# Optimization experiments

Measured on AMD Instinct MI355X. Metric: run time of the kernel, lower is better.

Reference implementation:

```python
import jax, jax.numpy as jnp
import numpy as np

WS = 7   # window size
SS = 3   # shift size


def _ln(x, g, b):
    m = x.mean(-1, keepdims=True)
    v = ((x - m) ** 2).mean(-1, keepdims=True)
    return (x - m) / jnp.sqrt(v + 1e-5) * g + b


def setup_inputs() -> dict:
    key = jax.random.key(0)
    ks = jax.random.split(key, 8)
    B, H, W, C, nh = 64, 56, 56, 96, 3
    N = WS * WS
    x = jax.random.normal(ks[0], (B, H * W, C), jnp.float32)

    # Swin SW-MSA attention mask: [nW, N, N], 0 where attention is allowed, -100 otherwise
    img = np.zeros((H, W), np.int32)
    cnt = 0
    for hs in (slice(0, H - WS), slice(H - WS, H - SS), slice(H - SS, None)):
        for wsl in (slice(0, W - WS), slice(W - WS, W - SS), slice(W - SS, None)):
            img[hs, wsl] = cnt
            cnt += 1
    win = img.reshape(H // WS, WS, W // WS, WS).transpose(0, 2, 1, 3).reshape(-1, N)
    am = np.where(win[:, None, :] != win[:, :, None], -100.0, 0.0).astype(np.float32)

    # relative position index: [N, N] in [0, (2*WS-1)^2)
    coords = np.stack(np.meshgrid(np.arange(WS), np.arange(WS), indexing='ij')).reshape(2, -1)
    rel = (coords[:, :, None] - coords[:, None, :]).transpose(1, 2, 0)
    rel[..., 0] += WS - 1
    rel[..., 1] += WS - 1
    rel[..., 0] *= 2 * WS - 1
    rel_index = jnp.asarray(rel.sum(-1), jnp.int32)

    p = lambda k, sh: jax.random.normal(k, sh, jnp.float32) * 0.02
    return dict(
        x=x,
        attn_mask=jnp.asarray(am),
        rel_index=rel_index,
        norm1_g=jnp.ones((C,), jnp.float32), norm1_b=jnp.zeros((C,), jnp.float32),
        qkv_w=p(ks[1], (3 * C, C)), qkv_b=jnp.zeros((3 * C,), jnp.float32),
        rel_bias_table=p(ks[2], ((2 * WS - 1) ** 2, nh)),
        proj_w=p(ks[3], (C, C)), proj_b=jnp.zeros((C,), jnp.float32),
        norm2_g=jnp.ones((C,), jnp.float32), norm2_b=jnp.zeros((C,), jnp.float32),
        fc1_w=p(ks[4], (4 * C, C)), fc1_b=jnp.zeros((4 * C,), jnp.float32),
        fc2_w=p(ks[5], (C, 4 * C)), fc2_b=jnp.zeros((C,), jnp.float32),
        H=56, W=56,
    )


def reference(x, attn_mask, rel_index, norm1_g, norm1_b, qkv_w, qkv_b,
              rel_bias_table, proj_w, proj_b, norm2_g, norm2_b,
              fc1_w, fc1_b, fc2_w, fc2_b, H, W):
    B, L, C = x.shape
    nh = rel_bias_table.shape[1]
    d = C // nh
    N = WS * WS
    shortcut = x

    xn = _ln(x, norm1_g, norm1_b).reshape(B, H, W, C)
    # cyclic shift (H%WS==0, W%WS==0 so no padding needed)
    xs = jnp.roll(xn, (-SS, -SS), axis=(1, 2))
    # window partition -> [B*nW, N, C]
    xw = xs.reshape(B, H // WS, WS, W // WS, WS, C).transpose(0, 1, 3, 2, 4, 5).reshape(-1, N, C)
    B_ = xw.shape[0]
    nW = attn_mask.shape[0]

    qkv = (xw @ qkv_w.T + qkv_b).reshape(B_, N, 3, nh, d).transpose(2, 0, 3, 1, 4)
    q, k, v = qkv[0] * (d ** -0.5), qkv[1], qkv[2]  # [B_, nh, N, d]
    attn = jnp.einsum('bhnd,bhmd->bhnm', q, k)
    bias = rel_bias_table[rel_index.reshape(-1)].reshape(N, N, nh).transpose(2, 0, 1)
    attn = attn + bias[None]
    attn = attn.reshape(B_ // nW, nW, nh, N, N) + attn_mask[None, :, None]
    attn = jax.nn.softmax(attn.reshape(B_, nh, N, N), axis=-1)
    out = jnp.einsum('bhnm,bhmd->bhnd', attn, v).transpose(0, 2, 1, 3).reshape(B_, N, C)
    out = out @ proj_w.T + proj_b

    # window reverse + reverse cyclic shift
    xr = out.reshape(B, H // WS, W // WS, WS, WS, C).transpose(0, 1, 3, 2, 4, 5).reshape(B, H, W, C)
    xr = jnp.roll(xr, (SS, SS), axis=(1, 2)).reshape(B, L, C)

    x = shortcut + xr
    h = _ln(x, norm2_g, norm2_b)
    h = jax.nn.gelu(h @ fc1_w.T + fc1_b, approximate=False) @ fc2_w.T + fc2_b
    return x + h
```

## Files before the change

### kernel.cpp

```cpp
#include <hip/hip_runtime.h>
#include <hip/hip_bf16.h>

typedef __attribute__((ext_vector_type(8))) short short8;
typedef __attribute__((ext_vector_type(4))) float f32x4;

constexpr int HW = 56;

constexpr int SR    = 104;
constexpr int SVT   = 200;
constexpr int OFF_X = 0;
constexpr int OFF_Q = 64 * SR;
constexpr int OFF_K = 2 * 64 * SR;
constexpr int OFF_V = 3 * 64 * SR;
constexpr int POOLN = OFF_V + 32 * SVT;

constexpr int WQKV  = 0;
constexpr int WPROJ = 27648;
constexpr int WFC1  = 36864;
constexpr int WFC2  = 73728;
constexpr int WTOT  = 110592;
constexpr int BIASN = 64 * 3 * 49 * 64;
constexpr size_t WS_M1 = (size_t)WTOT * 2;
constexpr size_t WS_M2 = WS_M1 + (size_t)BIASN * 4;

__device__ __forceinline__ ushort bfc(float f) {
  union { __hip_bfloat16 h; ushort u; } v;
  v.h = __float2bfloat16(f);
  return v.u;
}
__device__ __forceinline__ uint pk2(float a, float b) {
  union { __hip_bfloat162 h2; uint u; } v;
  v.h2 = __float22bfloat162_rn(make_float2(a, b));
  return v.u;
}
__device__ __forceinline__ void st4(short* p, float a, float b, float c, float d) {
  uint2 u; u.x = pk2(a, b); u.y = pk2(c, d);
  *(uint2*)p = u;
}
__device__ __forceinline__ short8 ldw8(const float* p) {
  float4 a = *(const float4*)p;
  float4 b = *(const float4*)(p + 4);
  short8 r;
  r[0] = (short)bfc(a.x); r[1] = (short)bfc(a.y); r[2] = (short)bfc(a.z); r[3] = (short)bfc(a.w);
  r[4] = (short)bfc(b.x); r[5] = (short)bfc(b.y); r[6] = (short)bfc(b.z); r[7] = (short)bfc(b.w);
  return r;
}
template<bool PRE>
__device__ __forceinline__ short8 wfrag(const short* wsb, int ts, int lane, const float* fsrc) {
  if constexpr (PRE) return *(const short8*)&wsb[(ts << 9) + lane * 8];
  else               return ldw8(fsrc);
}
__device__ __forceinline__ float gelu(float v) {
  return v * __builtin_amdgcn_rcpf(1.0f + __expf(-1.702f * v));
}
__device__ __forceinline__ void stage9(const short* g0, short* l0, int wv, int lane) {
  #pragma unroll
  for (int s4 = 0; s4 < 3; ++s4) {
    int s = wv + 4 * s4;
    if (s < 9)
      __builtin_amdgcn_global_load_lds((const unsigned int*)(g0 + (s << 9) + lane * 8),
                                       (unsigned int*)(l0 + (s << 9)), 16, 0, 0);
  }
}

__global__ __launch_bounds__(256) void cvt_weights(
    const float* __restrict__ qkv_w, const float* __restrict__ proj_w,
    const float* __restrict__ fc1_w, const float* __restrict__ fc2_w,
    short* __restrict__ ws)
{
  int idx = blockIdx.x * 256 + threadIdx.x;
  if (idx >= WTOT) return;
  int j = idx & 7, lane = (idx >> 3) & 63;
  int cl = lane & 15;
  int g  = 8 * (lane >> 4) + j;
  float v;
  if (idx < WPROJ) {
    int ts = idx >> 9; int tile = ts / 3, s = ts - 3 * tile;
    v = qkv_w[(size_t)(16 * tile + cl) * 96 + 32 * s + g];
    if (tile < 6) v *= 0.17677669529663687f;
  } else if (idx < WFC1) {
    int ts = (idx - WPROJ) >> 9; int tile = ts / 3, s = ts - 3 * tile;
    v = proj_w[(size_t)(16 * tile + cl) * 96 + 32 * s + g];
  } else if (idx < WFC2) {
    int ts = (idx - WFC1) >> 9; int T = ts / 3, s = ts - 3 * T;
    int cn = T / 6, nt = T - 6 * cn;
    v = fc1_w[(size_t)(96 * cn + 16 * nt + cl) * 96 + 32 * s + g];
  } else {
    int ts = (idx - WFC2) >> 9; int T = ts / 3, s = ts - 3 * T;
    int cn = T / 6, nt = T - 6 * cn;
    v = fc2_w[(size_t)(16 * nt + cl) * 384 + 96 * cn + 32 * s + g];
  }
  ws[idx] = (short)bfc(v);
}

__global__ __launch_bounds__(256) void prep_bias(
    const float* __restrict__ attn_mask, const int* __restrict__ rel_index,
    const float* __restrict__ rel_tab, float* __restrict__ bias3)
{
  int idx = blockIdx.x * 256 + threadIdx.x;
  if (idx >= BIASN) return;
  int k = idx & 63;
  int t = idx >> 6;
  int q = t % 49;
  int wh = t / 49;
  int h = wh % 3, w = wh / 3;
  float v = -1e30f;
  if (k < 49) {
    int qk = q * 49 + k;
    v = rel_tab[rel_index[qk] * 3 + h] + attn_mask[(size_t)w * 2401 + qk];
  }
  bias3[idx] = v;
}

template<int MODE>
__global__ __launch_bounds__(256, 3) void swin_mfma_kernel(
    const float* __restrict__ x,
    const float* __restrict__ attn_mask,
    const int*   __restrict__ rel_index,
    const float* __restrict__ n1g, const float* __restrict__ n1b,
    const float* __restrict__ qkv_w, const float* __restrict__ qkv_b,
    const float* __restrict__ rel_tab,
    const float* __restrict__ proj_w, const float* __restrict__ proj_b,
    const float* __restrict__ n2g, const float* __restrict__ n2b,
    const float* __restrict__ fc1_w, const float* __restrict__ fc1_b,
    const float* __restrict__ fc2_w, const float* __restrict__ fc2_b,
    const short* __restrict__ wsw,
    const float* __restrict__ bias3,
    float* __restrict__ out)
{
  constexpr bool PRE = (MODE >= 1);
  __shared__ alignas(16) short pool[POOLN];
  short* bufA = (short*)&pool[OFF_K];
  short* bufB = (short*)&pool[OFF_K + 4608];

  const int tid  = threadIdx.x;
  const int wv   = tid >> 6;
  const int lane = tid & 63;
  const int ln   = lane & 15;
  const int gq   = lane >> 4;
  const int bw   = blockIdx.x;
  const int b    = bw >> 6, widx = bw & 63;
  const int wr   = widx >> 3, wc = widx & 7;

  const f32x4 zf = {0.f, 0.f, 0.f, 0.f};
  const int qq = 16 * wv + ln;

  auto gbase = [&](int n) -> size_t {
    int i = n / 7, j = n - 7 * i;
    int h = wr * 7 + i + 3; if (h >= HW) h -= HW;
    int w = wc * 7 + j + 3; if (w >= HW) w -= HW;
    return ((size_t)b * (HW * HW) + (size_t)h * HW + w) * 96;
  };
  const size_t obase = gbase(qq < 49 ? qq : 48);

  float xraw[6][4];
  {
    if (qq < 49) {
      const float* xr = x + obase;
      #pragma unroll
      for (int nt = 0; nt < 6; ++nt) {
        float4 v = *(const float4*)&xr[16 * nt + 4 * gq];
        xraw[nt][0] = v.x; xraw[nt][1] = v.y; xraw[nt][2] = v.z; xraw[nt][3] = v.w;
      }
    } else {
      #pragma unroll
      for (int nt = 0; nt < 6; ++nt)
        xraw[nt][0] = xraw[nt][1] = xraw[nt][2] = xraw[nt][3] = 0.f;
    }
    float s1 = 0.f, s2 = 0.f;
    #pragma unroll
    for (int nt = 0; nt < 6; ++nt)
      #pragma unroll
      for (int r = 0; r < 4; ++r) { s1 += xraw[nt][r]; s2 += xraw[nt][r] * xraw[nt][r]; }
    s1 += __shfl_xor(s1, 16, 64); s1 += __shfl_xor(s1, 32, 64);
    s2 += __shfl_xor(s2, 16, 64); s2 += __shfl_xor(s2, 32, 64);
    float mean = s1 * (1.f / 96.f);
    float inv  = rsqrtf(s2 * (1.f / 96.f) - mean * mean + 1e-5f);
    #pragma unroll
    for (int nt = 0; nt < 6; ++nt) {
      float4 g4 = *(const float4*)&n1g[16 * nt + 4 * gq];
      float4 b4 = *(const float4*)&n1b[16 * nt + 4 * gq];
      st4(&pool[OFF_X + qq * SR + 16 * nt + 4 * gq],
          (xraw[nt][0] - mean) * inv * g4.x + b4.x,
          (xraw[nt][1] - mean) * inv * g4.y + b4.y,
          (xraw[nt][2] - mean) * inv * g4.z + b4.z,
          (xraw[nt][3] - mean) * inv * g4.w + b4.w);
    }
  }
  __syncthreads();

  {
    short8 af[3][4];
    #pragma unroll
    for (int s = 0; s < 3; ++s)
      #pragma unroll
      for (int m = 0; m < 4; ++m)
        af[s][m] = *(const short8*)&pool[OFF_X + (16 * m + ln) * SR + 32 * s + 8 * gq];

    const float sc_ = 0.17677669529663687f;
    for (int t = wv; t < 18; t += 4) {
      short8 wf[3];
      #pragma unroll
      for (int s = 0; s < 3; ++s)
        wf[s] = wfrag<PRE>(wsw + WQKV, t * 3 + s, lane,
                           qkv_w + (size_t)(16 * t + ln) * 96 + 32 * s + 8 * gq);
      int which = t / 6;
      if (which == 2) {
        int d  = 16 * (t - 12) + ln;
        float bv = qkv_b[192 + d];
        int dd = d & 31, hh = d >> 5;
        __builtin_amdgcn_s_setprio(1);
        #pragma unroll
        for (int m = 0; m < 4; ++m) {
          f32x4 acc = zf;
          #pragma unroll
          for (int s = 0; s < 3; ++s)
            acc = __builtin_amdgcn_mfma_f32_16x16x32_bf16(af[s][m], wf[s], acc, 0, 0, 0);
          st4(&pool[OFF_V + dd * SVT + hh * 64 + 16 * m + 4 * gq],
              acc[0] + bv, acc[1] + bv, acc[2] + bv, acc[3] + bv);
        }
        __builtin_amdgcn_s_setprio(0);
      } else {
        float4 b4 = *(const float4*)&qkv_b[16 * t + 4 * gq];
        if (which == 0) {
          if constexpr (PRE) { b4.x *= sc_; b4.y *= sc_; b4.z *= sc_; b4.w *= sc_; }
        }
        __builtin_amdgcn_s_setprio(1);
        #pragma unroll
        for (int m = 0; m < 4; ++m) {
          f32x4 acc = zf;
          #pragma unroll
          for (int s = 0; s < 3; ++s)
            acc = __builtin_amdgcn_mfma_f32_16x16x32_bf16(wf[s], af[s][m], acc, 0, 0, 0);
          int tok = 16 * m + ln;
          float v0 = acc[0] + b4.x, v1 = acc[1] + b4.y, v2 = acc[2] + b4.z, v3 = acc[3] + b4.w;
          if (which == 0) {
            if constexpr (PRE)
              st4(&pool[OFF_Q + tok * SR + 16 * t + 4 * gq], v0, v1, v2, v3);
            else
              st4(&pool[OFF_Q + tok * SR + 16 * t + 4 * gq], v0 * sc_, v1 * sc_, v2 * sc_, v3 * sc_);
          } else {
            st4(&pool[OFF_K + tok * SR + 16 * (t - 6) + 4 * gq], v0, v1, v2, v3);
          }
        }
        __builtin_amdgcn_s_setprio(0);
      }
    }
  }
  __syncthreads();

  const int qc = qq < 49 ? qq : 48;
  int   relvv[4][4];
  float maskb[4][4];
  if constexpr (MODE < 2) {
    #pragma unroll
    for (int nt = 0; nt < 4; ++nt)
      #pragma unroll
      for (int r = 0; r < 4; ++r) {
        int key = 16 * nt + 4 * gq + r;
        if (key < 49) {
          int qk = qc * 49 + key;
          relvv[nt][r] = rel_index[qk];
          maskb[nt][r] = attn_mask[(size_t)widx * 2401 + qk];
        } else {
          relvv[nt][r] = 0;
          maskb[nt][r] = -1e30f;
        }
      }
  }
  const float* bph = nullptr;
  if constexpr (MODE == 2) bph = bias3 + ((size_t)widx * 3 * 49 + qc) * 64;

  for (int h = 0; h < 3; ++h) {
    short8 bq = *(const short8*)&pool[OFF_Q + qq * SR + h * 32 + 8 * gq];
    f32x4 sc[4];
    __builtin_amdgcn_s_setprio(1);
    #pragma unroll
    for (int nt = 0; nt < 4; ++nt) {
      f32x4 bia;
      if constexpr (MODE == 2) {
        bia = *(const f32x4*)&bph[h * 3136 + 16 * nt + 4 * gq];
      } else {
        #pragma unroll
        for (int r = 0; r < 4; ++r)
          bia[r] = rel_tab[relvv[nt][r] * 3 + h] + maskb[nt][r];
      }
      short8 ak = *(const short8*)&pool[OFF_K + (16 * nt + ln) * SR + h * 32 + 8 * gq];
      sc[nt] = __builtin_amdgcn_mfma_f32_16x16x32_bf16(ak, bq, bia, 0, 0, 0);
    }
    __builtin_amdgcn_s_setprio(0);
    float pv[4][4];
    float sum = 0.f;
    #pragma unroll
    for (int nt = 0; nt < 4; ++nt)
      #pragma unroll
      for (int r = 0; r < 4; ++r) { pv[nt][r] = __expf(sc[nt][r]); sum += pv[nt][r]; }
    sum += __shfl_xor(sum, 16, 64);
    sum += __shfl_xor(sum, 32, 64);
    float inv = __builtin_amdgcn_rcpf(sum);
    #pragma unroll
    for (int nt = 0; nt < 4; ++nt)
      st4(&pool[OFF_X + qq * SR + 16 * nt + 4 * gq],
          pv[nt][0] * inv, pv[nt][1] * inv, pv[nt][2] * inv, pv[nt][3] * inv);

    short8 bp0 = *(const short8*)&pool[OFF_X + qq * SR + 8 * gq];
    short8 bp1 = *(const short8*)&pool[OFF_X + qq * SR + 32 + 8 * gq];
    __builtin_amdgcn_s_setprio(1);
    #pragma unroll
    for (int dt = 0; dt < 2; ++dt) {
      short8 av0 = *(const short8*)&pool[OFF_V + (16 * dt + ln) * SVT + h * 64 + 8 * gq];
      short8 av1 = *(const short8*)&pool[OFF_V + (16 * dt + ln) * SVT + h * 64 + 32 + 8 * gq];
      f32x4 o = __builtin_amdgcn_mfma_f32_16x16x32_bf16(av0, bp0, zf, 0, 0, 0);
      o = __builtin_amdgcn_mfma_f32_16x16x32_bf16(av1, bp1, o, 0, 0, 0);
      st4(&pool[OFF_Q + qq * SR + h * 32 + 16 * dt + 4 * gq], o[0], o[1], o[2], o[3]);
    }
    __builtin_amdgcn_s_setprio(0);
  }

  short8 ao[3];
  #pragma unroll
  for (int s = 0; s < 3; ++s)
    ao[s] = *(const short8*)&pool[OFF_Q + qq * SR + 32 * s + 8 * gq];
  __syncthreads();

  if constexpr (PRE) stage9(wsw + WPROJ, bufA, wv, lane);
  __syncthreads();

  if constexpr (PRE) stage9(wsw + WPROJ + 9 * 512, bufB, wv, lane);
  float y[6][4];
  __builtin_amdgcn_s_setprio(1);
  #pragma unroll
  for (int nt = 0; nt < 3; ++nt) {
    f32x4 acc = zf;
    #pragma unroll
    for (int s = 0; s < 3; ++s) {
      short8 wfr = PRE ? *(const short8*)&bufA[(nt * 3 + s) * 512 + lane * 8]
                       : ldw8(proj_w + (size_t)(16 * nt + ln) * 96 + 32 * s + 8 * gq);
      acc = __builtin_amdgcn_mfma_f32_16x16x32_bf16(wfr, ao[s], acc, 0, 0, 0);
    }
    float4 pb = *(const float4*)&proj_b[16 * nt + 4 * gq];
    y[nt][0] = acc[0] + pb.x + xraw[nt][0];
    y[nt][1] = acc[1] + pb.y + xraw[nt][1];
    y[nt][2] = acc[2] + pb.z + xraw[nt][2];
    y[nt][3] = acc[3] + pb.w + xraw[nt][3];
  }
  __builtin_amdgcn_s_setprio(0);
  __syncthreads();

  if constexpr (PRE) stage9(wsw + WFC1, bufA, wv, lane);
  __builtin_amdgcn_s_setprio(1);
  #pragma unroll
  for (int nt = 3; nt < 6; ++nt) {
    f32x4 acc = zf;
    #pragma unroll
    for (int s = 0; s < 3; ++s) {
      short8 wfr = PRE ? *(const short8*)&bufB[((nt - 3) * 3 + s) * 512 + lane * 8]
                       : ldw8(proj_w + (size_t)(16 * nt + ln) * 96 + 32 * s + 8 * gq);
      acc = __builtin_amdgcn_mfma_f32_16x16x32_bf16(wfr, ao[s], acc, 0, 0, 0);
    }
    float4 pb = *(const float4*)&proj_b[16 * nt + 4 * gq];
    y[nt][0] = acc[0] + pb.x + xraw[nt][0];
    y[nt][1] = acc[1] + pb.y + xraw[nt][1];
    y[nt][2] = acc[2] + pb.z + xraw[nt][2];
    y[nt][3] = acc[3] + pb.w + xraw[nt][3];
  }
  __builtin_amdgcn_s_setprio(0);
  {
    float s1 = 0.f, s2 = 0.f;
    #pragma unroll
    for (int nt = 0; nt < 6; ++nt)
      #pragma unroll
      for (int r = 0; r < 4; ++r) { s1 += y[nt][r]; s2 += y[nt][r] * y[nt][r]; }
    s1 += __shfl_xor(s1, 16, 64); s1 += __shfl_xor(s1, 32, 64);
    s2 += __shfl_xor(s2, 16, 64); s2 += __shfl_xor(s2, 32, 64);
    float mean = s1 * (1.f / 96.f);
    float inv  = rsqrtf(s2 * (1.f / 96.f) - mean * mean + 1e-5f);
    #pragma unroll
    for (int nt = 0; nt < 6; ++nt) {
      float4 g4 = *(const float4*)&n2g[16 * nt + 4 * gq];
      float4 b4 = *(const float4*)&n2b[16 * nt + 4 * gq];
      st4(&pool[OFF_Q + qq * SR + 16 * nt + 4 * gq],
          (y[nt][0] - mean) * inv * g4.x + b4.x,
          (y[nt][1] - mean) * inv * g4.y + b4.y,
          (y[nt][2] - mean) * inv * g4.z + b4.z,
          (y[nt][3] - mean) * inv * g4.w + b4.w);
    }
  }
  short8 ay[3];
  #pragma unroll
  for (int s = 0; s < 3; ++s)
    ay[s] = *(const short8*)&pool[OFF_Q + qq * SR + 32 * s + 8 * gq];
  __syncthreads();

  f32x4 accO[6] = {zf, zf, zf, zf, zf, zf};
  for (int cn = 0; cn < 4; ++cn) {
    if constexpr (PRE) stage9(wsw + WFC1 + (cn * 18 + 9) * 512, bufB, wv, lane);
    __builtin_amdgcn_s_setprio(1);
    #pragma unroll
    for (int nt = 0; nt < 3; ++nt) {
      f32x4 acc = zf;
      #pragma unroll
      for (int s = 0; s < 3; ++s) {
        short8 wfr = PRE ? *(const short8*)&bufA[(nt * 3 + s) * 512 + lane * 8]
                         : ldw8(fc1_w + (size_t)(96 * cn + 16 * nt + ln) * 96 + 32 * s + 8 * gq);
        acc = __builtin_amdgcn_mfma_f32_16x16x32_bf16(wfr, ay[s], acc, 0, 0, 0);
      }
      float4 b1 = *(const float4*)&fc1_b[96 * cn + 16 * nt + 4 * gq];
      st4(&pool[OFF_X + qq * SR + 16 * nt + 4 * gq],
          gelu(acc[0] + b1.x), gelu(acc[1] + b1.y),
          gelu(acc[2] + b1.z), gelu(acc[3] + b1.w));
    }
    __builtin_amdgcn_s_setprio(0);
    __syncthreads();
    if constexpr (PRE) stage9(wsw + WFC2 + (cn * 18) * 512, bufA, wv, lane);
    __builtin_amdgcn_s_setprio(1);
    #pragma unroll
    for (int nt = 3; nt < 6; ++nt) {
      f32x4 acc = zf;
      #pragma unroll
      for (int s = 0; s < 3; ++s) {
        short8 wfr = PRE ? *(const short8*)&bufB[((nt - 3) * 3 + s) * 512 + lane * 8]
                         : ldw8(fc1_w + (size_t)(96 * cn + 16 * nt + ln) * 96 + 32 * s + 8 * gq);
        acc = __builtin_amdgcn_mfma_f32_16x16x32_bf16(wfr, ay[s], acc, 0, 0, 0);
      }
      float4 b1 = *(const float4*)&fc1_b[96 * cn + 16 * nt + 4 * gq];
      st4(&pool[OFF_X + qq * SR + 16 * nt + 4 * gq],
          gelu(acc[0] + b1.x), gelu(acc[1] + b1.y),
          gelu(acc[2] + b1.z), gelu(acc[3] + b1.w));
    }
    __builtin_amdgcn_s_setprio(0);
    short8 ah[3];
    #pragma unroll
    for (int s = 0; s < 3; ++s)
      ah[s] = *(const short8*)&pool[OFF_X + qq * SR + 32 * s + 8 * gq];
    __syncthreads();
    if constexpr (PRE) stage9(wsw + WFC2 + (cn * 18 + 9) * 512, bufB, wv, lane);
    __builtin_amdgcn_s_setprio(1);
    #pragma unroll
    for (int nt = 0; nt < 3; ++nt) {
      #pragma unroll
      for (int s = 0; s < 3; ++s) {
        short8 wfr = PRE ? *(const short8*)&bufA[(nt * 3 + s) * 512 + lane * 8]
                         : ldw8(fc2_w + (size_t)(16 * nt + ln) * 384 + 96 * cn + 32 * s + 8 * gq);
        accO[nt] = __builtin_amdgcn_mfma_f32_16x16x32_bf16(wfr, ah[s], accO[nt], 0, 0, 0);
      }
    }
    __builtin_amdgcn_s_setprio(0);
    __syncthreads();
    if constexpr (PRE) { if (cn < 3) stage9(wsw + WFC1 + ((cn + 1) * 18) * 512, bufA, wv, lane); }
    __builtin_amdgcn_s_setprio(1);
    #pragma unroll
    for (int nt = 3; nt < 6; ++nt) {
      #pragma unroll
      for (int s = 0; s < 3; ++s) {
        short8 wfr = PRE ? *(const short8*)&bufB[((nt - 3) * 3 + s) * 512 + lane * 8]
                         : ldw8(fc2_w + (size_t)(16 * nt + ln) * 384 + 96 * cn + 32 * s + 8 * gq);
        accO[nt] = __builtin_amdgcn_mfma_f32_16x16x32_bf16(wfr, ah[s], accO[nt], 0, 0, 0);
      }
    }
    __builtin_amdgcn_s_setprio(0);
    __syncthreads();
  }

  if (qq < 49) {
    float* dst = out + obase;
    #pragma unroll
    for (int nt = 0; nt < 6; ++nt) {
      float4 fb = *(const float4*)&fc2_b[16 * nt + 4 * gq];
      float4 v;
      v.x = y[nt][0] + accO[nt][0] + fb.x;
      v.y = y[nt][1] + accO[nt][1] + fb.y;
      v.z = y[nt][2] + accO[nt][2] + fb.z;
      v.w = y[nt][3] + accO[nt][3] + fb.w;
      *(float4*)&dst[16 * nt + 4 * gq] = v;
    }
  }
}

extern "C" void kernel_launch(void* const* d_in, const int* in_sizes, int n_in,
                              void* d_out, int out_size, void* d_ws, size_t ws_size,
                              hipStream_t stream) {
  const float* x         = (const float*)d_in[0];
  const float* attn_mask = (const float*)d_in[1];
  const int*   rel_index = (const int*)  d_in[2];
  const float* n1g       = (const float*)d_in[3];
  const float* n1b       = (const float*)d_in[4];
  const float* qkv_w     = (const float*)d_in[5];
  const float* qkv_b     = (const float*)d_in[6];
  const float* rel_tab   = (const float*)d_in[7];
  const float* proj_w    = (const float*)d_in[8];
  const float* proj_b    = (const float*)d_in[9];
  const float* n2g       = (const float*)d_in[10];
  const float* n2b       = (const float*)d_in[11];
  const float* fc1_w     = (const float*)d_in[12];
  const float* fc1_b     = (const float*)d_in[13];
  const float* fc2_w     = (const float*)d_in[14];
  const float* fc2_b     = (const float*)d_in[15];
  float* out = (float*)d_out;

  const int B = in_sizes[0] / (HW * HW * 96);
  const bool m1 = ws_size >= WS_M1;
  const bool m2 = ws_size >= WS_M2;
  short* ws    = (short*)d_ws;
  float* bias3 = (float*)((char*)d_ws + WS_M1);

  if (m1)
    cvt_weights<<<(WTOT + 255) / 256, 256, 0, stream>>>(qkv_w, proj_w, fc1_w, fc2_w, ws);
  if (m2)
    prep_bias<<<(BIASN + 255) / 256, 256, 0, stream>>>(attn_mask, rel_index, rel_tab, bias3);

  if (m2)
    swin_mfma_kernel<2><<<B * 64, 256, 0, stream>>>(
        x, attn_mask, rel_index, n1g, n1b, qkv_w, qkv_b, rel_tab, proj_w, proj_b,
        n2g, n2b, fc1_w, fc1_b, fc2_w, fc2_b, (const short*)ws, (const float*)bias3, out);
  else if (m1)
    swin_mfma_kernel<1><<<B * 64, 256, 0, stream>>>(
        x, attn_mask, rel_index, n1g, n1b, qkv_w, qkv_b, rel_tab, proj_w, proj_b,
        n2g, n2b, fc1_w, fc1_b, fc2_w, fc2_b, (const short*)ws, (const float*)nullptr, out);
  else
    swin_mfma_kernel<0><<<B * 64, 256, 0, stream>>>(
        x, attn_mask, rel_index, n1g, n1b, qkv_w, qkv_b, rel_tab, proj_w, proj_b,
        n2g, n2b, fc1_w, fc1_b, fc2_w, fc2_b, (const short*)nullptr, (const float*)nullptr, out);
}
```

Measured before the change: 155.9 us.

## Repack MFMA outputs via shuffles and double-buffer full 18-tile weight stages

Replaces the LDS round trip for the softmax probabilities and the GELU hidden activations with in-register cross-lane shuffles that rebuild the bf16 B-operand fragments directly. Weight staging moves from 9-tile half buffers to full 18-tile buffers placed at two LDS regions, with each stage prefetching the next layer's weights. Each MLP chunk now runs FC1 and FC2 as whole phases, roughly halving the __syncthreads count. This trades LDS traffic and barriers for extra shuffle instructions and higher register pressure from holding six accumulators and the repacked fragments.

```diff
diff --git a/kernel.cpp b/kernel.cpp
--- a/kernel.cpp
+++ b/kernel.cpp
@@ -13,6 +13,10 @@
 constexpr int OFF_K = 2 * 64 * SR;
 constexpr int OFF_V = 3 * 64 * SR;
 constexpr int POOLN = OFF_V + 32 * SVT;
+constexpr int BUF0  = 0;
+constexpr int BUF1  = 9216;
+constexpr int YN    = OFF_V;
+constexpr int YSTR  = 96;
 
 constexpr int WQKV  = 0;
 constexpr int WPROJ = 27648;
@@ -53,11 +57,26 @@
 __device__ __forceinline__ float gelu(float v) {
   return v * __builtin_amdgcn_rcpf(1.0f + __expf(-1.702f * v));
 }
-__device__ __forceinline__ void stage9(const short* g0, short* l0, int wv, int lane) {
+__device__ __forceinline__ short8 repack(f32x4 A, f32x4 B, int ln, int gq) {
+  uint a_lo = pk2(A[0], A[1]), a_hi = pk2(A[2], A[3]);
+  uint b_lo = pk2(B[0], B[1]), b_hi = pk2(B[2], B[3]);
+  int s0 = ln + (((2 * gq)     & 3) << 4);
+  int s1 = ln + (((2 * gq + 1) & 3) << 4);
+  uint A0 = __shfl(a_lo, s0, 64), B0 = __shfl(b_lo, s0, 64);
+  uint A1 = __shfl(a_hi, s0, 64), B1 = __shfl(b_hi, s0, 64);
+  uint A2 = __shfl(a_lo, s1, 64), B2 = __shfl(b_lo, s1, 64);
+  uint A3 = __shfl(a_hi, s1, 64), B3 = __shfl(b_hi, s1, 64);
+  bool uA = (gq < 2);
+  union { uint u[4]; short8 s8; } r;
+  r.u[0] = uA ? A0 : B0; r.u[1] = uA ? A1 : B1;
+  r.u[2] = uA ? A2 : B2; r.u[3] = uA ? A3 : B3;
+  return r.s8;
+}
+__device__ __forceinline__ void stage18(const short* g0, short* l0, int wv, int lane) {
   #pragma unroll
-  for (int s4 = 0; s4 < 3; ++s4) {
-    int s = wv + 4 * s4;
-    if (s < 9)
+  for (int i = 0; i < 5; ++i) {
+    int s = wv + 4 * i;
+    if (s < 18)
       __builtin_amdgcn_global_load_lds((const unsigned int*)(g0 + (s << 9) + lane * 8),
                                        (unsigned int*)(l0 + (s << 9)), 16, 0, 0);
   }
@@ -130,8 +149,8 @@
 {
   constexpr bool PRE = (MODE >= 1);
   __shared__ alignas(16) short pool[POOLN];
-  short* bufA = (short*)&pool[OFF_K];
-  short* bufB = (short*)&pool[OFF_K + 4608];
+  short* buf0 = pool + BUF0;
+  short* buf1 = pool + BUF1;
 
   const int tid  = threadIdx.x;
   const int wv   = tid >> 6;
@@ -289,7 +308,7 @@
       sc[nt] = __builtin_amdgcn_mfma_f32_16x16x32_bf16(ak, bq, bia, 0, 0, 0);
     }
     __builtin_amdgcn_s_setprio(0);
-    float pv[4][4];
+    f32x4 pv[4];
     float sum = 0.f;
     #pragma unroll
     for (int nt = 0; nt < 4; ++nt)
@@ -300,11 +319,10 @@
     float inv = __builtin_amdgcn_rcpf(sum);
     #pragma unroll
     for (int nt = 0; nt < 4; ++nt)
-      st4(&pool[OFF_X + qq * SR + 16 * nt + 4 * gq],
-          pv[nt][0] * inv, pv[nt][1] * inv, pv[nt][2] * inv, pv[nt][3] * inv);
-
-    short8 bp0 = *(const short8*)&pool[OFF_X + qq * SR + 8 * gq];
-    short8 bp1 = *(const short8*)&pool[OFF_X + qq * SR + 32 + 8 * gq];
+      #pragma unroll
+      for (int r = 0; r < 4; ++r) pv[nt][r] *= inv;
+    short8 bp0 = repack(pv[0], pv[1], ln, gq);
+    short8 bp1 = repack(pv[2], pv[3], ln, gq);
     __builtin_amdgcn_s_setprio(1);
     #pragma unroll
     for (int dt = 0; dt < 2; ++dt) {
@@ -323,18 +341,18 @@
     ao[s] = *(const short8*)&pool[OFF_Q + qq * SR + 32 * s + 8 * gq];
   __syncthreads();
 
-  if constexpr (PRE) stage9(wsw + WPROJ, bufA, wv, lane);
+  if constexpr (PRE) stage18(wsw + WPROJ, buf0, wv, lane);
   __syncthreads();
 
-  if constexpr (PRE) stage9(wsw + WPROJ + 9 * 512, bufB, wv, lane);
+  if constexpr (PRE) stage18(wsw + WFC1, buf1, wv, lane);
   float y[6][4];
   __builtin_amdgcn_s_setprio(1);
   #pragma unroll
-  for (int nt = 0; nt < 3; ++nt) {
+  for (int nt = 0; nt < 6; ++nt) {
     f32x4 acc = zf;
     #pragma unroll
     for (int s = 0; s < 3; ++s) {
-      short8 wfr = PRE ? *(const short8*)&bufA[(nt * 3 + s) * 512 + lane * 8]
+      short8 wfr = PRE ? *(const short8*)&buf0[((nt * 3 + s) << 9) + lane * 8]
                        : ldw8(proj_w + (size_t)(16 * nt + ln) * 96 + 32 * s + 8 * gq);
       acc = __builtin_amdgcn_mfma_f32_16x16x32_bf16(wfr, ao[s], acc, 0, 0, 0);
     }
@@ -345,26 +363,6 @@
     y[nt][3] = acc[3] + pb.w + xraw[nt][3];
   }
   __builtin_amdgcn_s_setprio(0);
-  __syncthreads();
-
-  if constexpr (PRE) stage9(wsw + WFC1, bufA, wv, lane);
-  __builtin_amdgcn_s_setprio(1);
-  #pragma unroll
-  for (int nt = 3; nt < 6; ++nt) {
-    f32x4 acc = zf;
-    #pragma unroll
-    for (int s = 0; s < 3; ++s) {
-      short8 wfr = PRE ? *(const short8*)&bufB[((nt - 3) * 3 + s) * 512 + lane * 8]
-                       : ldw8(proj_w + (size_t)(16 * nt + ln) * 96 + 32 * s + 8 * gq);
-      acc = __builtin_amdgcn_mfma_f32_16x16x32_bf16(wfr, ao[s], acc, 0, 0, 0);
-    }
-    float4 pb = *(const float4*)&proj_b[16 * nt + 4 * gq];
-    y[nt][0] = acc[0] + pb.x + xraw[nt][0];
-    y[nt][1] = acc[1] + pb.y + xraw[nt][1];
-    y[nt][2] = acc[2] + pb.z + xraw[nt][2];
-    y[nt][3] = acc[3] + pb.w + xraw[nt][3];
-  }
-  __builtin_amdgcn_s_setprio(0);
   {
     float s1 = 0.f, s2 = 0.f;
     #pragma unroll
@@ -379,7 +377,7 @@
     for (int nt = 0; nt < 6; ++nt) {
       float4 g4 = *(const float4*)&n2g[16 * nt + 4 * gq];
       float4 b4 = *(const float4*)&n2b[16 * nt + 4 * gq];
-      st4(&pool[OFF_Q + qq * SR + 16 * nt + 4 * gq],
+      st4(&pool[YN + qq * YSTR + 16 * nt + 4 * gq],
           (y[nt][0] - mean) * inv * g4.x + b4.x,
           (y[nt][1] - mean) * inv * g4.y + b4.y,
           (y[nt][2] - mean) * inv * g4.z + b4.z,
@@ -389,77 +387,49 @@
   short8 ay[3];
   #pragma unroll
   for (int s = 0; s < 3; ++s)
-    ay[s] = *(const short8*)&pool[OFF_Q + qq * SR + 32 * s + 8 * gq];
+    ay[s] = *(const short8*)&pool[YN + qq * YSTR + 32 * s + 8 * gq];
   __syncthreads();
 
   f32x4 accO[6] = {zf, zf, zf, zf, zf, zf};
+  short8 hq[3];
+  #pragma unroll
   for (int cn = 0; cn < 4; ++cn) {
-    if constexpr (PRE) stage9(wsw + WFC1 + (cn * 18 + 9) * 512, bufB, wv, lane);
+    if constexpr (PRE) stage18(wsw + WFC2 + (cn * 18) * 512, buf0, wv, lane);
+    f32x4 ha[6];
     __builtin_amdgcn_s_setprio(1);
     #pragma unroll
-    for (int nt = 0; nt < 3; ++nt) {
+    for (int nt = 0; nt < 6; ++nt) {
       f32x4 acc = zf;
       #pragma unroll
       for (int s = 0; s < 3; ++s) {
-        short8 wfr = PRE ? *(const short8*)&bufA[(nt * 3 + s) * 512 + lane * 8]
+        short8 wfr = PRE ? *(const short8*)&buf1[((nt * 3 + s) << 9) + lane * 8]
                          : ldw8(fc1_w + (size_t)(96 * cn + 16 * nt + ln) * 96 + 32 * s + 8 * gq);
         acc = __builtin_amdgcn_mfma_f32_16x16x32_bf16(wfr, ay[s], acc, 0, 0, 0);
       }
       float4 b1 = *(const float4*)&fc1_b[96 * cn + 16 * nt + 4 * gq];
-      st4(&pool[OFF_X + qq * SR + 16 * nt + 4 * gq],
-          gelu(acc[0] + b1.x), gelu(acc[1] + b1.y),
-          gelu(acc[2] + b1.z), gelu(acc[3] + b1.w));
+      ha[nt][0] = gelu(acc[0] + b1.x);
+      ha[nt][1] = gelu(acc[1] + b1.y);
+      ha[nt][2] = gelu(acc[2] + b1.z);
+      ha[nt][3] = gelu(acc[3] + b1.w);
     }
     __builtin_amdgcn_s_setprio(0);
+    #pragma unroll
+    for (int s = 0; s < 3; ++s) hq[s] = repack(ha[2 * s], ha[2 * s + 1], ln, gq);
     __syncthreads();
-    if constexpr (PRE) stage9(wsw + WFC2 + (cn * 18) * 512, bufA, wv, lane);
+
+    if constexpr (PRE) { if (cn < 3) stage18(wsw + WFC1 + ((cn + 1) * 18) * 512, buf1, wv, lane); }
     __builtin_amdgcn_s_setprio(1);
     #pragma unroll
-    for (int nt = 3; nt < 6; ++nt) {
-      f32x4 acc = zf;
+    for (int nt = 0; nt < 6; ++nt) {
       #pragma unroll
       for (int s = 0; s < 3; ++s) {
-        short8 wfr = PRE ? *(const short8*)&bufB[((nt - 3) * 3 + s) * 512 + lane * 8]
-                         : ldw8(fc1_w + (size_t)(96 * cn + 16 * nt + ln) * 96 + 32 * s + 8 * gq);
-        acc = __builtin_amdgcn_mfma_f32_16x16x32_bf16(wfr, ay[s], acc, 0, 0, 0);
-      }
-      float4 b1 = *(const float4*)&fc1_b[96 * cn + 16 * nt + 4 * gq];
-      st4(&pool[OFF_X + qq * SR + 16 * nt + 4 * gq],
-          gelu(acc[0] + b1.x), gelu(acc[1] + b1.y),
-          gelu(acc[2] + b1.z), gelu(acc[3] + b1.w));
+        short8 wfr = PRE ? *(const short8*)&buf0[((nt * 3 + s) << 9) + lane * 8]
+                         : ldw8(fc2_w + (size_t)(16 * nt + ln) * 384 + 96 * cn + 32 * s + 8 * gq);
+        accO[nt] = __builtin_amdgcn_mfma_f32_16x16x32_bf16(wfr, hq[s], accO[nt], 0, 0, 0);
+      }
     }
     __builtin_amdgcn_s_setprio(0);
-    short8 ah[3];
-    #pragma unroll
-    for (int s = 0; s < 3; ++s)
-      ah[s] = *(const short8*)&pool[OFF_X + qq * SR + 32 * s + 8 * gq];
-    __syncthreads();
-    if constexpr (PRE) stage9(wsw + WFC2 + (cn * 18 + 9) * 512, bufB, wv, lane);
-    __builtin_amdgcn_s_setprio(1);
-    #pragma unroll
-    for (int nt = 0; nt < 3; ++nt) {
-      #pragma unroll
-      for (int s = 0; s < 3; ++s) {
-        short8 wfr = PRE ? *(const short8*)&bufA[(nt * 3 + s) * 512 + lane * 8]
-                         : ldw8(fc2_w + (size_t)(16 * nt + ln) * 384 + 96 * cn + 32 * s + 8 * gq);
-        accO[nt] = __builtin_amdgcn_mfma_f32_16x16x32_bf16(wfr, ah[s], accO[nt], 0, 0, 0);
-      }
-    }
-    __builtin_amdgcn_s_setprio(0);
-    __syncthreads();
-    if constexpr (PRE) { if (cn < 3) stage9(wsw + WFC1 + ((cn + 1) * 18) * 512, bufA, wv, lane); }
-    __builtin_amdgcn_s_setprio(1);
-    #pragma unroll
-    for (int nt = 3; nt < 6; ++nt) {
-      #pragma unroll
-      for (int s = 0; s < 3; ++s) {
-        short8 wfr = PRE ? *(const short8*)&bufB[((nt - 3) * 3 + s) * 512 + lane * 8]
-                         : ldw8(fc2_w + (size_t)(16 * nt + ln) * 384 + 96 * cn + 32 * s + 8 * gq);
-        accO[nt] = __builtin_amdgcn_mfma_f32_16x16x32_bf16(wfr, ah[s], accO[nt], 0, 0, 0);
-      }
-    }
-    __builtin_amdgcn_s_setprio(0);
-    __syncthreads();
+    if (cn < 3) __syncthreads();
   }
 
   if (qq < 49) {
```

Result: slower. 161.2 us (+3.4%).
